# Optimization experiments

Measured on AMD Instinct MI355X. Metric: run time of the kernel, lower is better.

Reference implementation:

```python
import jax, jax.numpy as jnp
import numpy as np
from jax import lax

B, H, W, C = 8, 72, 72, 16
HID_E, HID_P, T = 128, 16, 64
P_EPS = 1e-06
ALIVE_TH = 0.1

# Sobel kernels. The torch code runs conv on NCHW with spatial dims (D2, D1)
# (x.transpose(1,3)); in our NHWC layout spatial dims are (D1, D2), so the
# equivalent kernel is the transpose. With angle=0: w1 = dx, w2 = dy = dx.T.
_DX = np.outer([1.0, 2.0, 1.0], [-1.0, 0.0, 1.0]) / 8.0
_W1_EFF = _DX.T            # transpose of w1
_W2_EFF = _DX              # transpose of w2 (= dy.T)


def _depthwise(x, k2d):
    c = x.shape[-1]
    ker = jnp.tile(jnp.asarray(k2d, x.dtype)[:, :, None, None], (1, 1, 1, c))  # HWIO (3,3,1,C)
    return lax.conv_general_dilated(x, ker, (1, 1), 'SAME',
                                    feature_group_count=c,
                                    dimension_numbers=('NHWC', 'HWIO', 'NHWC'))


def _conv2d(x, w, b):
    y = lax.conv_general_dilated(x, w, (1, 1), 'SAME',
                                 dimension_numbers=('NHWC', 'HWIO', 'NHWC'))
    return y + b


def _maxpool3(a):  # a: (B,H,W)
    return lax.reduce_window(a, -jnp.inf, lax.max, (1, 3, 3), (1, 1, 1),
                             [(0, 0), (1, 1), (1, 1)])


def setup_inputs() -> dict:
    key = jax.random.key(0)
    ks = jax.random.split(key, 6)
    c3 = 3 * C
    x = jax.random.uniform(ks[0], (B, H, W, C), jnp.float32)
    conv1_w = jax.random.normal(ks[1], (3, 3, c3, HID_P), jnp.float32) * (1.0 / np.sqrt(9 * c3))
    conv1_b = jnp.zeros((HID_P,), jnp.float32)
    conv2_w = jax.random.normal(ks[2], (3, 3, HID_P, 1), jnp.float32) * (1.0 / np.sqrt(9 * HID_P))
    conv2_b = jnp.zeros((1,), jnp.float32)
    fc0_w = jax.random.normal(ks[3], (c3, HID_E), jnp.float32) * (1.0 / np.sqrt(c3))
    fc0_b = jnp.zeros((HID_E,), jnp.float32)
    fc1_w = jax.random.normal(ks[4], (HID_E, C), jnp.float32) * 0.01  # torch init is zeros; small random for a non-degenerate baseline
    return dict(x=x, conv1_w=conv1_w, conv1_b=conv1_b, conv2_w=conv2_w,
                conv2_b=conv2_b, fc0_w=fc0_w, fc0_b=fc0_b, fc1_w=fc1_w)


def reference(x, conv1_w, conv1_b, conv2_w, conv2_b, fc0_w, fc0_b, fc1_w):
    base_key = jax.random.key(42)

    def perceive(x):  # (B,H,W,C) -> (B,H,W,3C)
        return jnp.concatenate([x, _depthwise(x, _W1_EFF), _depthwise(x, _W2_EFF)], axis=-1)

    def lambda_net(perc):  # (B,H,W,3C) -> (B,H,W)
        h = jax.nn.relu(_conv2d(perc, conv1_w, conv1_b))
        return jax.nn.sigmoid(_conv2d(h, conv2_w, conv2_b))[..., 0]

    def alive(x):  # alpha channel index 3
        return _maxpool3(x[..., 3]) > ALIVE_TH

    def update(x, lambdas, key):
        pre = alive(x)
        perc = perceive(x)
        dx = jax.nn.relu(perc @ fc0_w + fc0_b) @ fc1_w  # pointwise MLP, fc1 has no bias
        upd = 1.0 - jax.random.bernoulli(key, lambdas).astype(x.dtype)  # (B,H,W)
        xn = x + dx * upd[..., None]
        life = (pre & alive(xn)).astype(x.dtype)[..., None]
        return xn * life, upd, perc

    # initial perceive/lambda/update (step 0)
    perc0 = perceive(x)
    lam0 = lambda_net(perc0)
    x0, upd0, perc = update(x, lam0, jax.random.fold_in(base_key, 0))
    un0 = jnp.ones((x.shape[0], H, W), x.dtype)

    def step(carry, n):
        xc, updc, percc, un = carry
        lam = lambda_net(percc)
        p_n = un * lam + P_EPS
        out = (xc, p_n, lam, updc)
        un = un * (1.0 - lam)
        xn, updn, percn = update(xc, lam, jax.random.fold_in(base_key, n))
        return (xn, updn, percn, un), out

    _, (x_steps, p_steps, lam_steps, upd_steps) = lax.scan(
        step, (x0, upd0, perc, un0), jnp.arange(1, T + 1))
    p_norm = p_steps / jnp.sum(p_steps, axis=0)
    return x_steps, p_norm, lam_steps, upd_steps
```

## Files before the change

### kernel.cpp

```cpp
#include <hip/hip_runtime.h>
#include <cstdint>
#include <cmath>

#define B_    8
#define H_    72
#define W_    72
#define C_    16
#define C3_   48
#define HP_   16
#define HE_   128
#define T_    64
#define NCELL 41472

typedef __attribute__((ext_vector_type(2))) double d2;

__host__ __device__ __forceinline__ void threefry2x32(uint32_t k0, uint32_t k1,
                                                      uint32_t& x0, uint32_t& x1) {
  uint32_t ks2 = k0 ^ k1 ^ 0x1BD11BDAu;
  x0 += k0; x1 += k1;
#define TF_R(r) { x0 += x1; x1 = (x1 << (r)) | (x1 >> (32 - (r))); x1 ^= x0; }
  TF_R(13) TF_R(15) TF_R(26) TF_R(6)
  x0 += k1; x1 += ks2 + 1u;
  TF_R(17) TF_R(29) TF_R(16) TF_R(24)
  x0 += ks2; x1 += k0 + 2u;
  TF_R(13) TF_R(15) TF_R(26) TF_R(6)
  x0 += k0; x1 += k1 + 3u;
  TF_R(17) TF_R(29) TF_R(16) TF_R(24)
  x0 += k1; x1 += ks2 + 4u;
  TF_R(13) TF_R(15) TF_R(26) TF_R(6)
  x0 += ks2; x1 += k0 + 5u;
#undef TF_R
}

__global__ void k_init(const float* __restrict__ xin, double* __restrict__ xA,
                       double* __restrict__ un) {
  int idx = blockIdx.x * 256 + threadIdx.x;
  if (idx < NCELL * C_) xA[idx] = (double)xin[idx];
  if (idx < NCELL) un[idx] = 1.0;
}

__global__ void k_prep(const float* __restrict__ w1, const float* __restrict__ f0w,
                       double* __restrict__ weffd, float* __restrict__ fc0tf) {
  int gid = blockIdx.x * 256 + threadIdx.x;
  const int stride = 26 * 256;
  for (int t = gid; t < 6400; t += stride) {
    int oc = t & 15;
    int c  = (t >> 4) & 15;
    int pos = t >> 8;
    int u = pos / 5, v = pos % 5;
    double acc = 0.0;
    for (int ei = 0; ei < 3; ei++) {
      int di = u - ei; if (di < 0 || di > 2) continue;
      for (int ej = 0; ej < 3; ej++) {
        int dj = v - ej; if (dj < 0 || dj > 2) continue;
        const float* wb = w1 + (size_t)((ei * 3 + ej) * C3_) * HP_ + oc;
        if (di == 1 && dj == 1) acc += (double)wb[c * HP_];
        double rf1 = (di == 0) ? -0.125 : (di == 2) ? 0.125 : 0.0;
        if (rf1 != 0.0) {
          double cf1 = (dj == 1) ? 2.0 : 1.0;
          acc += (double)wb[(C_ + c) * HP_] * (rf1 * cf1);
        }
        double cf2 = (dj == 0) ? -0.125 : (dj == 2) ? 0.125 : 0.0;
        if (cf2 != 0.0) {
          double rf2 = (di == 1) ? 2.0 : 1.0;
          acc += (double)wb[(2 * C_ + c) * HP_] * (cf2 * rf2);
        }
      }
    }
    weffd[t] = acc;
  }
  for (int t = gid; t < C3_ * HE_; t += stride) {
    int k = t >> 7, e = t & 127;
    fc0tf[e * C3_ + k] = f0w[t];
  }
}

__global__ void __launch_bounds__(512) k_conv1(const double* __restrict__ x,
    const double* __restrict__ weffd, const float* __restrict__ w1f,
    const float* __restrict__ b1f, double* __restrict__ hbuf) {
  __shared__ double sw[6400];
  for (int t = threadIdx.x; t < 6400; t += 512) sw[t] = weffd[t];
  __syncthreads();
  int oc = threadIdx.x & 15;
  int cs = threadIdx.x >> 4;
  int cell = blockIdx.x * 32 + cs;
  int j = cell % W_; int t2 = cell / W_; int i = t2 % H_; int b = t2 / H_;
  bool ring = (i == 0 || i == H_ - 1 || j == 0 || j == W_ - 1);
  double acc = (double)b1f[oc];
  if (!ring) {
#pragma unroll
    for (int p = 0; p < 25; p++) {
      const int u = p / 5, v = p % 5;
      int ii = i + u - 2, jj = j + v - 2;
      bool ok = ((unsigned)ii < (unsigned)H_) && ((unsigned)jj < (unsigned)W_);
      int iic = ok ? ii : 0;
      int jjc = ok ? jj : 0;
      const double* xp = x + (((size_t)((b * H_ + iic) * W_ + jjc)) << 4);
      const double* wp = sw + p * 256 + oc;
#pragma unroll
      for (int g = 0; g < 8; g++) {
        d2 xv = *(const d2*)(xp + 2 * g);
        double x0 = ok ? xv.x : 0.0;
        double x1 = ok ? xv.y : 0.0;
        acc = fma(x0, wp[(2 * g) * 16], acc);
        acc = fma(x1, wp[(2 * g + 1) * 16], acc);
      }
    }
  } else {
    for (int ei = 0; ei < 3; ei++) {
      int pi = i + ei - 1; if (pi < 0 || pi >= H_) continue;
      for (int ej = 0; ej < 3; ej++) {
        int pj = j + ej - 1; if (pj < 0 || pj >= W_) continue;
        const float* wb = w1f + (size_t)((ei * 3 + ej) * C3_) * HP_ + oc;
        for (int c = 0; c < C_; c++) {
          double v[3][3];
#pragma unroll
          for (int a2 = 0; a2 < 3; a2++) {
#pragma unroll
            for (int b2i = 0; b2i < 3; b2i++) {
              int ii2 = pi + a2 - 1, jj2 = pj + b2i - 1;
              bool ok = (ii2 >= 0 && ii2 < H_ && jj2 >= 0 && jj2 < W_);
              v[a2][b2i] = ok ? x[(((size_t)((b * H_ + ii2) * W_ + jj2)) << 4) + c] : 0.0;
            }
          }
          double ctr = v[1][1];
          double dw1 = (-v[0][0] - 2.0 * v[0][1] - v[0][2] + v[2][0] + 2.0 * v[2][1] + v[2][2]) * 0.125;
          double dw2 = (-v[0][0] + v[0][2] - 2.0 * v[1][0] + 2.0 * v[1][2] - v[2][0] + v[2][2]) * 0.125;
          acc += ctr * (double)wb[c * HP_] + dw1 * (double)wb[(C_ + c) * HP_] + dw2 * (double)wb[(2 * C_ + c) * HP_];
        }
      }
    }
  }
  hbuf[((size_t)cell << 4) + oc] = acc > 0.0 ? acc : 0.0;
}

__global__ void __launch_bounds__(256) k_upd(
    const double* __restrict__ x, const double* __restrict__ hbuf,
    const double* __restrict__ lamPrev, const float* __restrict__ fc0tf,
    const float* __restrict__ f1w, const float* __restrict__ w2f,
    const float* __restrict__ f0b, const float* __restrict__ b2,
    double* __restrict__ lamNext, double* __restrict__ xn,
    float* __restrict__ out_upd, double* __restrict__ un,
    float* __restrict__ out_lam, double* __restrict__ p_buf,
    uint32_t k0, uint32_t k1, int n) {
  __shared__ float s0f[HE_ * C3_];
  __shared__ float s1f[HE_ * C_];
  __shared__ float sw2[144];
  __shared__ float sb0[HE_];
  __shared__ double upool[3264];
  int tid = threadIdx.x;
  for (int t = tid; t < HE_ * C3_; t += 256) s0f[t] = fc0tf[t];
  for (int t = tid; t < HE_ * C_; t += 256) s1f[t] = f1w[t];
  if (tid < 144) sw2[tid] = w2f[tid];
  if (tid < HE_) sb0[tid] = f0b[tid];

  int lane = tid & 63;
  int wv = __builtin_amdgcn_readfirstlane(tid >> 6);
  int c0 = wv * 4;
  int cell = (blockIdx.x << 6) + lane;
  int j = cell % W_; int t2 = cell / W_; int i = t2 % H_; int b = t2 / H_;

  double pvx0 = 0.0, pvx1 = 0.0, pvx2 = 0.0, pvx3 = 0.0;
  double pw10 = 0.0, pw11 = 0.0, pw12 = 0.0, pw13 = 0.0;
  double pw20 = 0.0, pw21 = 0.0, pw22 = 0.0, pw23 = 0.0;
#pragma unroll
  for (int p = 0; p < 9; p++) {
    const int di = p / 3, dj = p % 3;
    const double k1c = (di == 0 ? -0.125 : di == 2 ? 0.125 : 0.0) * (dj == 1 ? 2.0 : 1.0);
    const double k2c = (dj == 0 ? -0.125 : dj == 2 ? 0.125 : 0.0) * (di == 1 ? 2.0 : 1.0);
    int ii = i + di - 1, jj = j + dj - 1;
    bool ok = ((unsigned)ii < (unsigned)H_) && ((unsigned)jj < (unsigned)W_);
    int iic = ok ? ii : 0;
    int jjc = ok ? jj : 0;
    const double* xp = x + (((size_t)((b * H_ + iic) * W_ + jjc)) << 4) + c0;
    d2 xa = *(const d2*)xp;
    d2 xb = *(const d2*)(xp + 2);
    double xv0 = ok ? xa.x : 0.0;
    double xv1 = ok ? xa.y : 0.0;
    double xv2 = ok ? xb.x : 0.0;
    double xv3 = ok ? xb.y : 0.0;
    if (p == 4) { pvx0 += xv0; pvx1 += xv1; pvx2 += xv2; pvx3 += xv3; }
    if (k1c != 0.0) {
      pw10 = fma(k1c, xv0, pw10); pw11 = fma(k1c, xv1, pw11);
      pw12 = fma(k1c, xv2, pw12); pw13 = fma(k1c, xv3, pw13);
    }
    if (k2c != 0.0) {
      pw20 = fma(k2c, xv0, pw20); pw21 = fma(k2c, xv1, pw21);
      pw22 = fma(k2c, xv2, pw22); pw23 = fma(k2c, xv3, pw23);
    }
  }
  {
    double* pr = upool + lane * 51;
    pr[c0 + 0] = pvx0; pr[c0 + 1] = pvx1; pr[c0 + 2] = pvx2; pr[c0 + 3] = pvx3;
    pr[16 + c0 + 0] = pw10; pr[16 + c0 + 1] = pw11; pr[16 + c0 + 2] = pw12; pr[16 + c0 + 3] = pw13;
    pr[32 + c0 + 0] = pw20; pr[32 + c0 + 1] = pw21; pr[32 + c0 + 2] = pw22; pr[32 + c0 + 3] = pw23;
  }
  __syncthreads();

  double z = (wv == 0) ? (double)b2[0] : 0.0;
  for (int di = 0; di < 3; di++) {
    int ii = i + di - 1; if (ii < 0 || ii >= H_) continue;
    for (int dj = 0; dj < 3; dj++) {
      int jj = j + dj - 1; if (jj < 0 || jj >= W_) continue;
      const double* hh = hbuf + (((size_t)((b * H_ + ii) * W_ + jj)) << 4) + c0;
      const float* ww = sw2 + (di * 3 + dj) * HP_ + c0;
      d2 h0 = *(const d2*)hh;
      d2 h1 = *(const d2*)(hh + 2);
      z = fma(h0.x, (double)ww[0], z);
      z = fma(h0.y, (double)ww[1], z);
      z = fma(h1.x, (double)ww[2], z);
      z = fma(h1.y, (double)ww[3], z);
    }
  }

  double pv[C3_];
#pragma unroll
  for (int k = 0; k < C3_; k++) pv[k] = upool[lane * 51 + k];

  double dx[C_];
#pragma unroll
  for (int c = 0; c < C_; c++) dx[c] = 0.0;
  int ebase = wv << 5;
#pragma unroll 1
  for (int eg = 0; eg < 32; eg += 4) {
    int e = ebase + eg;
    const float* w0 = s0f + e * C3_;
    double a0 = (double)sb0[e + 0];
    double a1 = (double)sb0[e + 1];
    double a2 = (double)sb0[e + 2];
    double a3 = (double)sb0[e + 3];
#pragma unroll
    for (int k = 0; k < C3_; k++) {
      a0 = fma(pv[k], (double)w0[k], a0);
      a1 = fma(pv[k], (double)w0[C3_ + k], a1);
      a2 = fma(pv[k], (double)w0[2 * C3_ + k], a2);
      a3 = fma(pv[k], (double)w0[3 * C3_ + k], a3);
    }
    a0 = a0 > 0.0 ? a0 : 0.0;
    a1 = a1 > 0.0 ? a1 : 0.0;
    a2 = a2 > 0.0 ? a2 : 0.0;
    a3 = a3 > 0.0 ? a3 : 0.0;
    const float* v0 = s1f + (e << 4);
#pragma unroll
    for (int c = 0; c < C_; c++) {
      double s = fma(a0, (double)v0[c], dx[c]);
      s = fma(a1, (double)v0[16 + c], s);
      s = fma(a2, (double)v0[32 + c], s);
      s = fma(a3, (double)v0[48 + c], s);
      dx[c] = s;
    }
  }

  __syncthreads();
  if (wv != 0) {
    double* pr = upool + (wv - 1) * 1088 + lane * 17;
#pragma unroll
    for (int c = 0; c < C_; c++) pr[c] = dx[c];
    pr[16] = z;
  }
  __syncthreads();
  if (wv != 0) return;

#pragma unroll
  for (int w = 0; w < 3; w++) {
    const double* pr = upool + w * 1088 + lane * 17;
#pragma unroll
    for (int c = 0; c < C_; c++) dx[c] += pr[c];
    z += pr[16];
  }

  double lamF = 1.0 / (1.0 + exp(-z));
  lamNext[cell] = lamF;
  double l = (n == 0) ? lamF : lamPrev[cell];

  if (n >= 1) {
    size_t o = (size_t)(n - 1) * NCELL + cell;
    out_lam[o] = (float)l;
    double u = un[cell];
    p_buf[o] = u * l + 1e-6;
    un[cell] = u * (1.0 - l);
  }

  uint32_t r0 = 0u, r1 = (uint32_t)cell;
  threefry2x32(k0, k1, r0, r1);
  double uf = (double)(r0 ^ r1) * 0x1p-32;
  double upd = (uf < l) ? 0.0 : 1.0;
  out_upd[(size_t)n * NCELL + cell] = (float)upd;
  const double* xc = x + ((size_t)cell << 4);
  double* xo = xn + ((size_t)cell << 4);
#pragma unroll
  for (int c = 0; c < C_; c++) xo[c] = xc[c] + dx[c] * upd;
}

__global__ void k_life(const double* __restrict__ xold, const double* __restrict__ xn,
                       double* __restrict__ xout, float* __restrict__ out_x, int n) {
  int idx = blockIdx.x * 256 + threadIdx.x;
  int c = idx & 15;
  int cell = idx >> 4;
  int j = cell % W_; int t = cell / W_; int i = t % H_; int b = t / H_;
  double mo = -1e300, mn2 = -1e300;
  for (int di = -1; di <= 1; di++) {
    int ii = i + di; if (ii < 0 || ii >= H_) continue;
    for (int dj = -1; dj <= 1; dj++) {
      int jj = j + dj; if (jj < 0 || jj >= W_) continue;
      size_t nb = (size_t)((b * H_ + ii) * W_ + jj) * C_;
      double a0 = xold[nb + 3]; if (a0 > mo) mo = a0;
      double a1 = xn[nb + 3];   if (a1 > mn2) mn2 = a1;
    }
  }
  bool life = (mo > 0.1) && (mn2 > 0.1);
  double v = life ? xn[((size_t)cell << 4) + c] : 0.0;
  xout[((size_t)cell << 4) + c] = v;
  out_x[(size_t)n * NCELL * C_ + ((size_t)cell << 4) + c] = (float)v;
}

__global__ void k_emit(const double* __restrict__ lam, const double* __restrict__ un,
                       float* __restrict__ out_lam, double* __restrict__ p_buf) {
  int cell = blockIdx.x * 256 + threadIdx.x;
  double l = lam[cell];
  size_t o = (size_t)(T_ - 1) * NCELL + cell;
  out_lam[o] = (float)l;
  p_buf[o] = un[cell] * l + 1e-6;
}

__global__ void k_pnorm(const double* __restrict__ p_buf, float* __restrict__ out_p) {
  int cell = blockIdx.x * 256 + threadIdx.x;
  double s = 0.0;
  for (int t = 0; t < T_; t++) s += p_buf[(size_t)t * NCELL + cell];
  for (int t = 0; t < T_; t++)
    out_p[(size_t)t * NCELL + cell] = (float)(p_buf[(size_t)t * NCELL + cell] / s);
}

extern "C" void kernel_launch(void* const* d_in, const int* in_sizes, int n_in,
                              void* d_out, int out_size, void* d_ws, size_t ws_size,
                              hipStream_t stream) {
  const float* xin = (const float*)d_in[0];
  const float* w1  = (const float*)d_in[1];
  const float* b1  = (const float*)d_in[2];
  const float* w2  = (const float*)d_in[3];
  const float* b2  = (const float*)d_in[4];
  const float* f0w = (const float*)d_in[5];
  const float* f0b = (const float*)d_in[6];
  const float* f1w = (const float*)d_in[7];

  float* out     = (float*)d_out;
  float* out_x   = out;
  float* out_p   = out_x + (size_t)T_ * NCELL * C_;
  float* out_lam = out_p + (size_t)T_ * NCELL;
  float* out_upd = out_lam + (size_t)T_ * NCELL;

  double* ws    = (double*)d_ws;
  double* xA    = ws;
  double* xB    = xA + (size_t)NCELL * C_;
  double* xn    = xB + (size_t)NCELL * C_;
  double* hbuf  = xn + (size_t)NCELL * C_;
  double* lamA  = hbuf + (size_t)NCELL * HP_;
  double* lamB  = lamA + NCELL;
  double* un    = lamB + NCELL;
  double* p_buf = un + NCELL;
  double* weffd = p_buf + (size_t)T_ * NCELL;
  float*  fc0tf = (float*)(weffd + 6400);

  k_init<<<2592, 256, 0, stream>>>(xin, xA, un);
  k_prep<<<26, 256, 0, stream>>>(w1, f0w, weffd, fc0tf);

  double* cur = lamA;
  double* nxt = lamB;

  for (int n = 0; n <= T_ - 1; n++) {
    k_conv1<<<1296, 512, 0, stream>>>(xA, weffd, w1, b1, hbuf);
    uint32_t kx0 = 0u, kx1 = (uint32_t)n;
    threefry2x32(0u, 42u, kx0, kx1);
    k_upd<<<648, 256, 0, stream>>>(xA, hbuf, cur, fc0tf, f1w, w2, f0b, b2,
                                   (n == 0 ? cur : nxt), xn, out_upd, un,
                                   out_lam, p_buf, kx0, kx1, n);
    k_life<<<2592, 256, 0, stream>>>(xA, xn, xB, out_x, n);
    { double* t = xA; xA = xB; xB = t; }
    if (n >= 1) { double* t = cur; cur = nxt; nxt = t; }
  }

  k_emit<<<162, 256, 0, stream>>>(cur, un, out_lam, p_buf);
  k_pnorm<<<162, 256, 0, stream>>>(p_buf, out_p);
}
```

Baseline: 15.49 ms.

## Tile conv1 input rows in shared memory and widen k_upd to eight waves

k_conv1 now handles half an image row per block and stages a 5x40x16 input halo tile in LDS. Each thread computes two output channels from that tile, using paired vector weight loads and even/odd accumulators to break the FMA dependency chain. This cuts redundant global loads of the 5x5 neighbourhood. k_upd goes from 256 to 512 threads, splitting the hidden-unit MLP loop and the perception channels across eight waves, with an extra LDS reduction stage. The cost is more LDS per block and more barriers, which may lower occupancy.

```diff
diff --git a/kernel.cpp b/kernel.cpp
--- a/kernel.cpp
+++ b/kernel.cpp
@@ -75,43 +75,71 @@
   }
 }
 
-__global__ void __launch_bounds__(512) k_conv1(const double* __restrict__ x,
+__global__ void __launch_bounds__(288) k_conv1(const double* __restrict__ x,
     const double* __restrict__ weffd, const float* __restrict__ w1f,
     const float* __restrict__ b1f, double* __restrict__ hbuf) {
   __shared__ double sw[6400];
-  for (int t = threadIdx.x; t < 6400; t += 512) sw[t] = weffd[t];
-  __syncthreads();
-  int oc = threadIdx.x & 15;
-  int cs = threadIdx.x >> 4;
-  int cell = blockIdx.x * 32 + cs;
-  int j = cell % W_; int t2 = cell / W_; int i = t2 % H_; int b = t2 / H_;
+  __shared__ double sx[3200];
+  int tid = threadIdx.x;
+  int bid = blockIdx.x;
+  int h = bid & 1;
+  int t2 = bid >> 1;
+  int i = t2 % H_;
+  int b = t2 / H_;
+  int j0 = h * 36;
+  for (int t = tid; t < 6400; t += 288) sw[t] = weffd[t];
+  for (int e = tid; e < 1600; e += 288) {
+    int icp = e & 7;
+    int col = (e >> 3) % 40;
+    int u = e / 320;
+    int ii = i + u - 2;
+    int jj = j0 - 2 + col;
+    bool ok = ((unsigned)ii < (unsigned)H_) && ((unsigned)jj < (unsigned)W_);
+    int iic = ok ? ii : 0, jjc = ok ? jj : 0;
+    const double* src = x + (((size_t)((b * H_ + iic) * W_ + jjc)) << 4) + 2 * icp;
+    d2 v = *(const d2*)src;
+    sx[e * 2]     = ok ? v.x : 0.0;
+    sx[e * 2 + 1] = ok ? v.y : 0.0;
+  }
+  __syncthreads();
+
+  int ocp = tid & 7;
+  int cs = tid >> 3;
+  int j = j0 + cs;
+  int cell = (b * H_ + i) * W_ + j;
+  int oc0 = 2 * ocp;
+  double bv0 = (double)b1f[oc0], bv1 = (double)b1f[oc0 + 1];
   bool ring = (i == 0 || i == H_ - 1 || j == 0 || j == W_ - 1);
-  double acc = (double)b1f[oc];
+  double r0, r1;
   if (!ring) {
+    double aE0 = bv0, aE1 = bv1, aO0 = 0.0, aO1 = 0.0;
 #pragma unroll
     for (int p = 0; p < 25; p++) {
       const int u = p / 5, v = p % 5;
-      int ii = i + u - 2, jj = j + v - 2;
-      bool ok = ((unsigned)ii < (unsigned)H_) && ((unsigned)jj < (unsigned)W_);
-      int iic = ok ? ii : 0;
-      int jjc = ok ? jj : 0;
-      const double* xp = x + (((size_t)((b * H_ + iic) * W_ + jjc)) << 4);
-      const double* wp = sw + p * 256 + oc;
+      const double* xr = sx + (u * 40 + cs + v) * 16;
+      const double* wp = sw + p * 256 + oc0;
 #pragma unroll
       for (int g = 0; g < 8; g++) {
-        d2 xv = *(const d2*)(xp + 2 * g);
-        double x0 = ok ? xv.x : 0.0;
-        double x1 = ok ? xv.y : 0.0;
-        acc = fma(x0, wp[(2 * g) * 16], acc);
-        acc = fma(x1, wp[(2 * g + 1) * 16], acc);
+        d2 xv = *(const d2*)(xr + 2 * g);
+        d2 w0 = *(const d2*)(wp + (2 * g) * 16);
+        d2 w1 = *(const d2*)(wp + (2 * g + 1) * 16);
+        if (p & 1) {
+          aO0 = fma(xv.x, w0.x, aO0); aO1 = fma(xv.x, w0.y, aO1);
+          aO0 = fma(xv.y, w1.x, aO0); aO1 = fma(xv.y, w1.y, aO1);
+        } else {
+          aE0 = fma(xv.x, w0.x, aE0); aE1 = fma(xv.x, w0.y, aE1);
+          aE0 = fma(xv.y, w1.x, aE0); aE1 = fma(xv.y, w1.y, aE1);
+        }
       }
     }
+    r0 = aE0 + aO0; r1 = aE1 + aO1;
   } else {
+    double acc0 = bv0, acc1 = bv1;
     for (int ei = 0; ei < 3; ei++) {
       int pi = i + ei - 1; if (pi < 0 || pi >= H_) continue;
       for (int ej = 0; ej < 3; ej++) {
         int pj = j + ej - 1; if (pj < 0 || pj >= W_) continue;
-        const float* wb = w1f + (size_t)((ei * 3 + ej) * C3_) * HP_ + oc;
+        const float* wb = w1f + (size_t)((ei * 3 + ej) * C3_) * HP_ + oc0;
         for (int c = 0; c < C_; c++) {
           double v[3][3];
 #pragma unroll
@@ -126,15 +154,19 @@
           double ctr = v[1][1];
           double dw1 = (-v[0][0] - 2.0 * v[0][1] - v[0][2] + v[2][0] + 2.0 * v[2][1] + v[2][2]) * 0.125;
           double dw2 = (-v[0][0] + v[0][2] - 2.0 * v[1][0] + 2.0 * v[1][2] - v[2][0] + v[2][2]) * 0.125;
-          acc += ctr * (double)wb[c * HP_] + dw1 * (double)wb[(C_ + c) * HP_] + dw2 * (double)wb[(2 * C_ + c) * HP_];
+          acc0 += ctr * (double)wb[c * HP_]     + dw1 * (double)wb[(C_ + c) * HP_]     + dw2 * (double)wb[(2 * C_ + c) * HP_];
+          acc1 += ctr * (double)wb[c * HP_ + 1] + dw1 * (double)wb[(C_ + c) * HP_ + 1] + dw2 * (double)wb[(2 * C_ + c) * HP_ + 1];
         }
       }
     }
-  }
-  hbuf[((size_t)cell << 4) + oc] = acc > 0.0 ? acc : 0.0;
-}
-
-__global__ void __launch_bounds__(256) k_upd(
+    r0 = acc0; r1 = acc1;
+  }
+  double* hp = hbuf + ((size_t)cell << 4) + oc0;
+  hp[0] = r0 > 0.0 ? r0 : 0.0;
+  hp[1] = r1 > 0.0 ? r1 : 0.0;
+}
+
+__global__ void __launch_bounds__(512) k_upd(
     const double* __restrict__ x, const double* __restrict__ hbuf,
     const double* __restrict__ lamPrev, const float* __restrict__ fc0tf,
     const float* __restrict__ f1w, const float* __restrict__ w2f,
@@ -147,22 +179,21 @@
   __shared__ float s1f[HE_ * C_];
   __shared__ float sw2[144];
   __shared__ float sb0[HE_];
-  __shared__ double upool[3264];
+  __shared__ double upool[4352];
   int tid = threadIdx.x;
-  for (int t = tid; t < HE_ * C3_; t += 256) s0f[t] = fc0tf[t];
-  for (int t = tid; t < HE_ * C_; t += 256) s1f[t] = f1w[t];
+  for (int t = tid; t < HE_ * C3_; t += 512) s0f[t] = fc0tf[t];
+  for (int t = tid; t < HE_ * C_; t += 512) s1f[t] = f1w[t];
   if (tid < 144) sw2[tid] = w2f[tid];
   if (tid < HE_) sb0[tid] = f0b[tid];
 
   int lane = tid & 63;
   int wv = __builtin_amdgcn_readfirstlane(tid >> 6);
-  int c0 = wv * 4;
   int cell = (blockIdx.x << 6) + lane;
   int j = cell % W_; int t2 = cell / W_; int i = t2 % H_; int b = t2 / H_;
 
-  double pvx0 = 0.0, pvx1 = 0.0, pvx2 = 0.0, pvx3 = 0.0;
-  double pw10 = 0.0, pw11 = 0.0, pw12 = 0.0, pw13 = 0.0;
-  double pw20 = 0.0, pw21 = 0.0, pw22 = 0.0, pw23 = 0.0;
+  int c0 = wv * 2;
+  double pA = 0.0, pB = 0.0;
+  double q1A = 0.0, q1B = 0.0, q2A = 0.0, q2B = 0.0;
 #pragma unroll
   for (int p = 0; p < 9; p++) {
     const int di = p / 3, dj = p % 3;
@@ -174,42 +205,36 @@
     int jjc = ok ? jj : 0;
     const double* xp = x + (((size_t)((b * H_ + iic) * W_ + jjc)) << 4) + c0;
     d2 xa = *(const d2*)xp;
-    d2 xb = *(const d2*)(xp + 2);
     double xv0 = ok ? xa.x : 0.0;
     double xv1 = ok ? xa.y : 0.0;
-    double xv2 = ok ? xb.x : 0.0;
-    double xv3 = ok ? xb.y : 0.0;
-    if (p == 4) { pvx0 += xv0; pvx1 += xv1; pvx2 += xv2; pvx3 += xv3; }
-    if (k1c != 0.0) {
-      pw10 = fma(k1c, xv0, pw10); pw11 = fma(k1c, xv1, pw11);
-      pw12 = fma(k1c, xv2, pw12); pw13 = fma(k1c, xv3, pw13);
-    }
-    if (k2c != 0.0) {
-      pw20 = fma(k2c, xv0, pw20); pw21 = fma(k2c, xv1, pw21);
-      pw22 = fma(k2c, xv2, pw22); pw23 = fma(k2c, xv3, pw23);
-    }
+    if (p == 4) { pA += xv0; pB += xv1; }
+    if (k1c != 0.0) { q1A = fma(k1c, xv0, q1A); q1B = fma(k1c, xv1, q1B); }
+    if (k2c != 0.0) { q2A = fma(k2c, xv0, q2A); q2B = fma(k2c, xv1, q2B); }
   }
   {
     double* pr = upool + lane * 51;
-    pr[c0 + 0] = pvx0; pr[c0 + 1] = pvx1; pr[c0 + 2] = pvx2; pr[c0 + 3] = pvx3;
-    pr[16 + c0 + 0] = pw10; pr[16 + c0 + 1] = pw11; pr[16 + c0 + 2] = pw12; pr[16 + c0 + 3] = pw13;
-    pr[32 + c0 + 0] = pw20; pr[32 + c0 + 1] = pw21; pr[32 + c0 + 2] = pw22; pr[32 + c0 + 3] = pw23;
+    pr[c0] = pA; pr[c0 + 1] = pB;
+    pr[16 + c0] = q1A; pr[16 + c0 + 1] = q1B;
+    pr[32 + c0] = q2A; pr[32 + c0 + 1] = q2B;
   }
   __syncthreads();
 
   double z = (wv == 0) ? (double)b2[0] : 0.0;
-  for (int di = 0; di < 3; di++) {
-    int ii = i + di - 1; if (ii < 0 || ii >= H_) continue;
-    for (int dj = 0; dj < 3; dj++) {
-      int jj = j + dj - 1; if (jj < 0 || jj >= W_) continue;
-      const double* hh = hbuf + (((size_t)((b * H_ + ii) * W_ + jj)) << 4) + c0;
-      const float* ww = sw2 + (di * 3 + dj) * HP_ + c0;
-      d2 h0 = *(const d2*)hh;
-      d2 h1 = *(const d2*)(hh + 2);
-      z = fma(h0.x, (double)ww[0], z);
-      z = fma(h0.y, (double)ww[1], z);
-      z = fma(h1.x, (double)ww[2], z);
-      z = fma(h1.y, (double)ww[3], z);
+  if (wv < 4) {
+    int cq = wv * 4;
+    for (int di = 0; di < 3; di++) {
+      int ii = i + di - 1; if (ii < 0 || ii >= H_) continue;
+      for (int dj = 0; dj < 3; dj++) {
+        int jj = j + dj - 1; if (jj < 0 || jj >= W_) continue;
+        const double* hh = hbuf + (((size_t)((b * H_ + ii) * W_ + jj)) << 4) + cq;
+        const float* ww = sw2 + (di * 3 + dj) * HP_ + cq;
+        d2 h0 = *(const d2*)hh;
+        d2 h1 = *(const d2*)(hh + 2);
+        z = fma(h0.x, (double)ww[0], z);
+        z = fma(h0.y, (double)ww[1], z);
+        z = fma(h1.x, (double)ww[2], z);
+        z = fma(h1.y, (double)ww[3], z);
+      }
     }
   }
 
@@ -220,9 +245,9 @@
   double dx[C_];
 #pragma unroll
   for (int c = 0; c < C_; c++) dx[c] = 0.0;
-  int ebase = wv << 5;
+  int ebase = wv << 4;
 #pragma unroll 1
-  for (int eg = 0; eg < 32; eg += 4) {
+  for (int eg = 0; eg < 16; eg += 4) {
     int e = ebase + eg;
     const float* w0 = s0f + e * C3_;
     double a0 = (double)sb0[e + 0];
@@ -252,7 +277,19 @@
   }
 
   __syncthreads();
-  if (wv != 0) {
+  if (wv >= 4) {
+    double* pr = upool + (wv - 4) * 1088 + lane * 17;
+#pragma unroll
+    for (int c = 0; c < C_; c++) pr[c] = dx[c];
+  }
+  __syncthreads();
+  if (wv < 4) {
+    const double* pr = upool + wv * 1088 + lane * 17;
+#pragma unroll
+    for (int c = 0; c < C_; c++) dx[c] += pr[c];
+  }
+  __syncthreads();
+  if (wv >= 1 && wv < 4) {
     double* pr = upool + (wv - 1) * 1088 + lane * 17;
 #pragma unroll
     for (int c = 0; c < C_; c++) pr[c] = dx[c];
@@ -368,10 +405,10 @@
   double* nxt = lamB;
 
   for (int n = 0; n <= T_ - 1; n++) {
-    k_conv1<<<1296, 512, 0, stream>>>(xA, weffd, w1, b1, hbuf);
+    k_conv1<<<1152, 288, 0, stream>>>(xA, weffd, w1, b1, hbuf);
     uint32_t kx0 = 0u, kx1 = (uint32_t)n;
     threefry2x32(0u, 42u, kx0, kx1);
-    k_upd<<<648, 256, 0, stream>>>(xA, hbuf, cur, fc0tf, f1w, w2, f0b, b2,
+    k_upd<<<648, 512, 0, stream>>>(xA, hbuf, cur, fc0tf, f1w, w2, f0b, b2,
                                    (n == 0 ? cur : nxt), xn, out_upd, un,
                                    out_lam, p_buf, kx0, kx1, n);
     k_life<<<2592, 256, 0, stream>>>(xA, xn, xB, out_x, n);
```

New measurement: 17.19 ms. +11.0%, slower.
